# Performance work log

Hardware: AMD Instinct MI355X
Metric: run time of the kernel (lower is better)

Reference implementation:

```python
import jax, jax.numpy as jnp
import numpy as np

N = 100000          # nodes per node type (paper, author)
E = 250000          # edges per relation
D_IN = 128          # input feature dim
H, C = 4, 32        # heads, channels per head (h_dim = H*C = 128)
HD = H * C
OUT = 349           # num classes
RELS = ["c", "w", "wb"]  # cites(paper->paper), writes(author->paper), written_by(paper->author)


def setup_inputs() -> dict:
    key = jax.random.key(0)
    ks = iter(jax.random.split(key, 64))
    def nrm(shape, scale=0.1):
        return jax.random.normal(next(ks), shape, jnp.float32) * scale
    inp = {
        "x_paper": jax.random.normal(next(ks), (N, D_IN), jnp.float32),
        "x_author": jax.random.normal(next(ks), (N, D_IN), jnp.float32),
        "ei_cites": jax.random.randint(next(ks), (2, E), 0, N),
        "ei_writes": jax.random.randint(next(ks), (2, E), 0, N),
        "ei_written": jax.random.randint(next(ks), (2, E), 0, N),
    }
    for l, din in [(0, D_IN), (1, HD)]:
        for r in RELS:
            inp[f"W{l}_{r}"] = nrm((din, HD))
            inp[f"as{l}_{r}"] = nrm((H, C))
            inp[f"ad{l}_{r}"] = nrm((H, C))
            inp[f"b{l}_{r}"] = jnp.zeros((HD,), jnp.float32)
    inp["lin_W"] = nrm((HD, OUT))
    inp["lin_b"] = jnp.zeros((OUT,), jnp.float32)
    return inp


def _gat_conv(x_src, x_dst, ei, W, att_s, att_d, b, n_dst):
    """PyG GATConv (concat heads, add_self_loops=False, shared lin for src/dst)."""
    h_s = (x_src @ W).reshape(-1, H, C)              # [Ns,H,C]
    h_d = (x_dst @ W).reshape(-1, H, C)              # [Nd,H,C]
    a_s = (h_s * att_s).sum(-1)                      # [Ns,H]
    a_d = (h_d * att_d).sum(-1)                      # [Nd,H]
    src, dst = ei[0], ei[1]
    e = jax.nn.leaky_relu(a_s[src] + a_d[dst], 0.2)  # [E,H]
    # segment softmax over incoming edges per dst node
    m = jax.ops.segment_max(e, dst, num_segments=n_dst)
    m = jnp.where(jnp.isfinite(m), m, 0.0)
    w = jnp.exp(e - m[dst])
    z = jax.ops.segment_sum(w, dst, num_segments=n_dst)
    alpha = w / (z[dst] + 1e-16)                     # [E,H]
    msg = h_s[src] * alpha[..., None]                # [E,H,C]
    agg = jax.ops.segment_sum(msg, dst, num_segments=n_dst)
    return agg.reshape(n_dst, HD) + b


def _forward(x_paper, x_author, ei_cites, ei_writes, ei_written, params, lin_W, lin_b):
    xp, xa = x_paper, x_author
    for l in range(2):
        p = params[l]
        # HeteroConv with sum aggregation across relations per dst node type
        op = _gat_conv(xp, xp, ei_cites, *p["c"], N) + _gat_conv(xa, xp, ei_writes, *p["w"], N)
        oa = _gat_conv(xp, xa, ei_written, *p["wb"], N)
        xp, xa = op, oa
        if l != 1:
            xp = jax.nn.leaky_relu(xp, 0.01)  # F.leaky_relu default slope
            xa = jax.nn.leaky_relu(xa, 0.01)
            # dropout: identity in eval/reference mode
    return xp @ lin_W + lin_b  # [N, OUT]


def reference(x_paper, x_author,
              W0_c, as0_c, ad0_c, b0_c, W0_w, as0_w, ad0_w, b0_w, W0_wb, as0_wb, ad0_wb, b0_wb,
              W1_c, as1_c, ad1_c, b1_c, W1_w, as1_w, ad1_w, b1_w, W1_wb, as1_wb, ad1_wb, b1_wb,
              lin_W, lin_b, ei_cites, ei_writes, ei_written):
    params = [
        {"c": (W0_c, as0_c, ad0_c, b0_c), "w": (W0_w, as0_w, ad0_w, b0_w), "wb": (W0_wb, as0_wb, ad0_wb, b0_wb)},
        {"c": (W1_c, as1_c, ad1_c, b1_c), "w": (W1_w, as1_w, ad1_w, b1_w), "wb": (W1_wb, as1_wb, ad1_wb, b1_wb)},
    ]
    return _forward(x_paper, x_author, ei_cites, ei_writes, ei_written, params, lin_W, lin_b)
```

## Files before the change

kernel.cpp:

```cpp
#include <hip/hip_runtime.h>

#define NN 100000
#define EE 250000
#define CAP 32

typedef unsigned int u32;
typedef unsigned short ushort;
typedef __attribute__((ext_vector_type(8))) short bf16x8;
typedef __attribute__((ext_vector_type(4))) float f32x4;

__device__ __forceinline__ ushort f2bf(float x) {
    u32 u = __float_as_uint(x);
    return (ushort)((u + 0x7fffu + ((u >> 16) & 1u)) >> 16);
}
__device__ __forceinline__ float bf2f(ushort h) {
    return __uint_as_float(((u32)h) << 16);
}

__global__ __launch_bounds__(256) void gemm_att(
    const float* __restrict__ X, const float* __restrict__ W,
    const float* __restrict__ atts, const float* __restrict__ attd,
    float* __restrict__ H, float* __restrict__ aS, float* __restrict__ aD)
{
    __shared__ float sW[64 * 128];
    __shared__ float sXT[128 * 32];
    const int tid = threadIdx.x;
    const size_t r0 = (size_t)blockIdx.x * 32;

    {
        int rl = tid & 31, kg = tid >> 5;
        const float4* Xr = (const float4*)(X + (r0 + rl) * 128);
#pragma unroll
        for (int t = 0; t < 4; ++t) {
            float4 u = Xr[kg * 4 + t];
            int k = kg * 16 + t * 4;
            sXT[(k + 0) * 32 + rl] = u.x;
            sXT[(k + 1) * 32 + rl] = u.y;
            sXT[(k + 2) * 32 + rl] = u.z;
            sXT[(k + 3) * 32 + rl] = u.w;
        }
    }

    const int jg = tid & 31;
    const int rg = tid >> 5;
    float acc[4][4] = {};

    for (int kh = 0; kh < 2; ++kh) {
        __syncthreads();
        const float4* Wu = (const float4*)(W + kh * 64 * 128);
        float4* sWv = (float4*)sW;
#pragma unroll
        for (int t = 0; t < 8; ++t)
            sWv[tid + 256 * t] = Wu[tid + 256 * t];
        __syncthreads();
#pragma unroll 4
        for (int k = 0; k < 64; ++k) {
            const float4 w = ((const float4*)sW)[k * 32 + jg];
            const int kk = kh * 64 + k;
            const float4 x = ((const float4*)sXT)[kk * 8 + rg];
            acc[0][0] += w.x * x.x; acc[0][1] += w.y * x.x; acc[0][2] += w.z * x.x; acc[0][3] += w.w * x.x;
            acc[1][0] += w.x * x.y; acc[1][1] += w.y * x.y; acc[1][2] += w.z * x.y; acc[1][3] += w.w * x.y;
            acc[2][0] += w.x * x.z; acc[2][1] += w.y * x.z; acc[2][2] += w.z * x.z; acc[2][3] += w.w * x.z;
            acc[3][0] += w.x * x.w; acc[3][1] += w.y * x.w; acc[3][2] += w.z * x.w; acc[3][3] += w.w * x.w;
        }
    }

    const float4 sv = ((const float4*)atts)[jg];
    const float4 dv = ((const float4*)attd)[jg];
    const int h = jg >> 3;

#pragma unroll
    for (int i = 0; i < 4; ++i) {
        const size_t row = r0 + rg * 4 + i;
        if (H)
            ((float4*)H)[row * 32 + jg] = make_float4(acc[i][0], acc[i][1], acc[i][2], acc[i][3]);
        float ps = acc[i][0] * sv.x + acc[i][1] * sv.y + acc[i][2] * sv.z + acc[i][3] * sv.w;
        float pd = acc[i][0] * dv.x + acc[i][1] * dv.y + acc[i][2] * dv.z + acc[i][3] * dv.w;
        ps += __shfl_xor(ps, 1); ps += __shfl_xor(ps, 2); ps += __shfl_xor(ps, 4);
        pd += __shfl_xor(pd, 1); pd += __shfl_xor(pd, 2); pd += __shfl_xor(pd, 4);
        if ((jg & 7) == 0) {
            aS[row * 4 + h] = ps;
            aD[row * 4 + h] = pd;
        }
    }
}

__global__ __launch_bounds__(256) void fold_w3(
    const float* __restrict__ W0, const float* __restrict__ a0,
    const float* __restrict__ W1, const float* __restrict__ a1,
    const float* __restrict__ W2, const float* __restrict__ a2,
    float* __restrict__ Wf)
{
    int i = blockIdx.x * 256 + threadIdx.x;
    if (i >= 1536) return;
    int r = i >> 9, j = i & 511;
    int k = j >> 2, h = j & 3;
    const float* W = (r == 0) ? W0 : (r == 1) ? W1 : W2;
    const float* a = (r == 0) ? a0 : (r == 1) ? a1 : a2;
    float s = 0.f;
#pragma unroll
    for (int c = 0; c < 32; ++c)
        s += W[k * 128 + h * 32 + c] * a[h * 32 + c];
    Wf[i] = s;
}

__global__ __launch_bounds__(256) void gemv_att(
    const float* __restrict__ X, const float* __restrict__ Wf,
    float* __restrict__ aD)
{
    __shared__ float sWf[512];
    const int tid = threadIdx.x;
    if (tid < 128)
        ((float4*)sWf)[tid] = ((const float4*)Wf)[tid];
    __syncthreads();
    const int t = blockIdx.x * 256 + tid;
    const int n = t >> 5, lane = t & 31;
    if (n >= NN) return;
    const float4 x = ((const float4*)X)[(size_t)n * 32 + lane];
    const float4 w0 = ((const float4*)sWf)[lane * 4 + 0];
    const float4 w1 = ((const float4*)sWf)[lane * 4 + 1];
    const float4 w2 = ((const float4*)sWf)[lane * 4 + 2];
    const float4 w3 = ((const float4*)sWf)[lane * 4 + 3];
    float p0 = x.x * w0.x + x.y * w1.x + x.z * w2.x + x.w * w3.x;
    float p1 = x.x * w0.y + x.y * w1.y + x.z * w2.y + x.w * w3.y;
    float p2 = x.x * w0.z + x.y * w1.z + x.z * w2.z + x.w * w3.z;
    float p3 = x.x * w0.w + x.y * w1.w + x.z * w2.w + x.w * w3.w;
#pragma unroll
    for (int off = 1; off < 32; off <<= 1) {
        p0 += __shfl_xor(p0, off);
        p1 += __shfl_xor(p1, off);
        p2 += __shfl_xor(p2, off);
        p3 += __shfl_xor(p3, off);
    }
    if (lane == 0)
        ((float4*)aD)[n] = make_float4(p0, p1, p2, p3);
}

__global__ __launch_bounds__(256) void fill_buckets(
    const int* __restrict__ ei, int* __restrict__ deg, int* __restrict__ bkt)
{
    int e = blockIdx.x * 256 + threadIdx.x;
    if (e >= EE) return;
    int s = ei[e], d = ei[EE + e];
    int slot = atomicAdd(&deg[d], 1);
    if (slot >= 0 && slot < CAP) bkt[(size_t)d * CAP + slot] = s;
}

__global__ __launch_bounds__(256) void aggregate(
    const int* __restrict__ deg, const int* __restrict__ bkt,
    const float* __restrict__ aS, const float* __restrict__ aD,
    const float* __restrict__ Hs, float* __restrict__ out,
    int accumulate, const float* __restrict__ b1, const float* __restrict__ b2,
    int act)
{
    int t = blockIdx.x * 256 + threadIdx.x;
    int d = t >> 5, lane = t & 31;
    if (d >= NN) return;
    int g = deg[d]; if (g > CAP) g = CAP; if (g < 0) g = 0;
    const int h = lane >> 3;
    const float adh = aD[d * 4 + h];
    const int* mybkt = bkt + (size_t)d * CAP;

    const int4 sa = *(const int4*)mybkt;
    const int4 sb = *(const int4*)(mybkt + 4);
    int sidx[8] = {sa.x, sa.y, sa.z, sa.w, sb.x, sb.y, sb.z, sb.w};
#pragma unroll
    for (int j = 0; j < 8; ++j)
        sidx[j] = (j < g) ? sidx[j] : 0;

    float e[8];
#pragma unroll
    for (int j = 0; j < 8; ++j) {
        float ev = aS[sidx[j] * 4 + h] + adh;
        e[j] = ev > 0.f ? ev : 0.2f * ev;
    }
    float m = -INFINITY;
#pragma unroll
    for (int j = 0; j < 8; ++j)
        if (j < g) m = fmaxf(m, e[j]);
    for (int j = 8; j < g; ++j) {
        int s = mybkt[j];
        float ev = aS[s * 4 + h] + adh;
        ev = ev > 0.f ? ev : 0.2f * ev;
        m = fmaxf(m, ev);
    }

    float4 acc = make_float4(0.f, 0.f, 0.f, 0.f);
    float z = 0.f;
#pragma unroll
    for (int j = 0; j < 8; ++j) {
        if (j < g) {
            float w = __expf(e[j] - m);
            z += w;
            float4 hv = ((const float4*)Hs)[(size_t)sidx[j] * 32 + lane];
            acc.x += w * hv.x; acc.y += w * hv.y; acc.z += w * hv.z; acc.w += w * hv.w;
        }
    }
    for (int j = 8; j < g; ++j) {
        int s = mybkt[j];
        float ev = aS[s * 4 + h] + adh;
        ev = ev > 0.f ? ev : 0.2f * ev;
        float w = __expf(ev - m);
        z += w;
        float4 hv = ((const float4*)Hs)[(size_t)s * 32 + lane];
        acc.x += w * hv.x; acc.y += w * hv.y; acc.z += w * hv.z; acc.w += w * hv.w;
    }
    float inv = 1.f / (z + 1e-16f);
    acc.x *= inv; acc.y *= inv; acc.z *= inv; acc.w *= inv;

    if (accumulate) {
        float4 p = ((const float4*)out)[(size_t)d * 32 + lane];
        acc.x += p.x; acc.y += p.y; acc.z += p.z; acc.w += p.w;
    }
    if (b1) {
        float4 bv = ((const float4*)b1)[lane];
        acc.x += bv.x; acc.y += bv.y; acc.z += bv.z; acc.w += bv.w;
    }
    if (b2) {
        float4 bv = ((const float4*)b2)[lane];
        acc.x += bv.x; acc.y += bv.y; acc.z += bv.z; acc.w += bv.w;
    }
    if (act) {
        acc.x = acc.x > 0.f ? acc.x : 0.01f * acc.x;
        acc.y = acc.y > 0.f ? acc.y : 0.01f * acc.y;
        acc.z = acc.z > 0.f ? acc.z : 0.01f * acc.z;
        acc.w = acc.w > 0.f ? acc.w : 0.01f * acc.w;
    }
    ((float4*)out)[(size_t)d * 32 + lane] = acc;
}

__global__ __launch_bounds__(256) void pad_w(
    const float* __restrict__ Wl, const float* __restrict__ bl,
    ushort* __restrict__ Whi, ushort* __restrict__ Wlo, float* __restrict__ bp)
{
    int i = blockIdx.x * 256 + threadIdx.x;
    if (i >= 384 * 128) return;
    int n = i >> 7, k = i & 127;
    float w = (n < 349) ? Wl[k * 349 + n] : 0.0f;
    ushort h = f2bf(w);
    Whi[i] = h;
    Wlo[i] = f2bf(w - bf2f(h));
    if (i < 384) bp[i] = (i < 349) ? bl[i] : 0.0f;
}

__global__ __launch_bounds__(256) void gemm_out(
    const float* __restrict__ X, const ushort* __restrict__ Whi,
    const ushort* __restrict__ Wlo, const float* __restrict__ bp,
    float* __restrict__ out)
{
    __shared__ ushort sAhi[64 * 128];
    __shared__ ushort sAlo[64 * 128];
    const int tid = threadIdx.x;
    const size_t r0 = (size_t)blockIdx.x * 64;

    {
        const int rl = tid >> 2, sub = tid & 3;
        const size_t row = r0 + rl;
        const float4* Xr = (const float4*)(X + row * 128);
        const u32 swz = ((u32)(rl & 7)) << 4;
        const float4 z4 = make_float4(0.f, 0.f, 0.f, 0.f);
#pragma unroll
        for (int i = 0; i < 4; ++i) {
            float4 u0 = (row < NN) ? Xr[sub * 8 + 2 * i] : z4;
            float4 u1 = (row < NN) ? Xr[sub * 8 + 2 * i + 1] : z4;
            float v[8] = {u0.x, u0.y, u0.z, u0.w, u1.x, u1.y, u1.z, u1.w};
            bf16x8 h8, l8;
#pragma unroll
            for (int e = 0; e < 8; ++e) {
                ushort h = f2bf(v[e]);
                h8[e] = (short)h;
                l8[e] = (short)f2bf(v[e] - bf2f(h));
            }
            u32 byteoff = ((u32)rl * 256u + (u32)((sub * 32 + i * 8) * 2)) ^ swz;
            *(bf16x8*)((char*)sAhi + byteoff) = h8;
            *(bf16x8*)((char*)sAlo + byteoff) = l8;
        }
    }
    __syncthreads();

    const int wave = tid >> 6, lane = tid & 63;
    const int lr = lane & 15;
    const int lg = lane >> 4;
    const int ncol0 = wave * 96;

    f32x4 acc[4][6];
#pragma unroll
    for (int mt = 0; mt < 4; ++mt)
#pragma unroll
        for (int nt = 0; nt < 6; ++nt)
            acc[mt][nt] = (f32x4){0.f, 0.f, 0.f, 0.f};

    for (int ks = 0; ks < 4; ++ks) {
        bf16x8 ah[4], al[4];
#pragma unroll
        for (int mt = 0; mt < 4; ++mt) {
            const int row = mt * 16 + lr;
            u32 byteoff = ((u32)row * 256u + (u32)(ks * 64 + lg * 16))
                          ^ (((u32)(row & 7)) << 4);
            ah[mt] = *(const bf16x8*)((const char*)sAhi + byteoff);
            al[mt] = *(const bf16x8*)((const char*)sAlo + byteoff);
        }
        bf16x8 bh[6], bl6[6];
#pragma unroll
        for (int nt = 0; nt < 6; ++nt) {
            const int n = ncol0 + nt * 16 + lr;
            const size_t off = (size_t)n * 128 + ks * 32 + lg * 8;
            bh[nt]  = *(const bf16x8*)(Whi + off);
            bl6[nt] = *(const bf16x8*)(Wlo + off);
        }
#pragma unroll
        for (int mt = 0; mt < 4; ++mt)
#pragma unroll
            for (int nt = 0; nt < 6; ++nt) {
                acc[mt][nt] = __builtin_amdgcn_mfma_f32_16x16x32_bf16(
                    ah[mt], bh[nt], acc[mt][nt], 0, 0, 0);
                acc[mt][nt] = __builtin_amdgcn_mfma_f32_16x16x32_bf16(
                    ah[mt], bl6[nt], acc[mt][nt], 0, 0, 0);
                acc[mt][nt] = __builtin_amdgcn_mfma_f32_16x16x32_bf16(
                    al[mt], bh[nt], acc[mt][nt], 0, 0, 0);
            }
    }

#pragma unroll
    for (int nt = 0; nt < 6; ++nt) {
        const int n = ncol0 + nt * 16 + lr;
        if (n >= 349) continue;
        const float bb = bp[n];
#pragma unroll
        for (int mt = 0; mt < 4; ++mt) {
#pragma unroll
            for (int r = 0; r < 4; ++r) {
                const size_t row = r0 + mt * 16 + lg * 4 + r;
                if (row < NN)
                    out[row * 349 + n] = acc[mt][nt][r] + bb;
            }
        }
    }
}

extern "C" void kernel_launch(void* const* d_in, const int* in_sizes, int n_in,
                              void* d_out, int out_size, void* d_ws, size_t ws_size,
                              hipStream_t stream)
{
    (void)in_sizes; (void)n_in; (void)out_size; (void)ws_size;
    const float* xp = (const float*)d_in[0];
    const float* xa = (const float*)d_in[1];
    const int* eic = (const int*)d_in[2];
    const int* eiw = (const int*)d_in[3];
    const int* eiwb = (const int*)d_in[4];
    auto Wl = [&](int l, int r) { return (const float*)d_in[5 + (l * 3 + r) * 4 + 0]; };
    auto As = [&](int l, int r) { return (const float*)d_in[5 + (l * 3 + r) * 4 + 1]; };
    auto Ad = [&](int l, int r) { return (const float*)d_in[5 + (l * 3 + r) * 4 + 2]; };
    auto Bs = [&](int l, int r) { return (const float*)d_in[5 + (l * 3 + r) * 4 + 3]; };
    const float* linW = (const float*)d_in[29];
    const float* linb = (const float*)d_in[30];

    char* wsp = (char*)d_ws;
    auto carve = [&](size_t bytes) -> void* {
        void* p = (void*)wsp;
        wsp += (bytes + 255) & ~(size_t)255;
        return p;
    };
    float* Hs = (float*)carve((size_t)NN * 128 * 4);
    float* P1 = (float*)carve((size_t)NN * 128 * 4);
    float* A1 = (float*)carve((size_t)NN * 128 * 4);
    float* P2 = (float*)carve((size_t)NN * 128 * 4);
    int* deg = (int*)carve((size_t)NN * 3 * 4);
    int* deg_c = deg, *deg_w = deg + NN, *deg_wb = deg + 2 * NN;
    int* bkt_c = (int*)carve((size_t)NN * CAP * 4);
    int* bkt_w = (int*)carve((size_t)NN * CAP * 4);
    int* bkt_wb = (int*)carve((size_t)NN * CAP * 4);
    float* aS = (float*)carve((size_t)NN * 4 * 4);
    float* aD = (float*)carve((size_t)NN * 4 * 4);
    float* aX = (float*)carve((size_t)NN * 4 * 4);
    ushort* Whi = (ushort*)carve((size_t)384 * 128 * 2);
    ushort* Wlo = (ushort*)carve((size_t)384 * 128 * 2);
    float* bp = (float*)carve((size_t)384 * 4);
    float* Wf = (float*)carve((size_t)3 * 512 * 4);

    dim3 blk(256);
    const int gG = NN / 32;
    const int gE = (EE + 255) / 256;
    const int gA = NN * 32 / 256;
    const int gO = (NN + 63) / 64;

    hipMemsetAsync(deg, 0, (size_t)NN * 3 * 4, stream);
    fill_buckets<<<gE, blk, 0, stream>>>(eic, deg_c, bkt_c);
    fill_buckets<<<gE, blk, 0, stream>>>(eiw, deg_w, bkt_w);
    fill_buckets<<<gE, blk, 0, stream>>>(eiwb, deg_wb, bkt_wb);
    fold_w3<<<6, blk, 0, stream>>>(Wl(0, 2), Ad(0, 2), Wl(0, 1), Ad(0, 1),
                                   Wl(1, 1), Ad(1, 1), Wf);

    gemm_att<<<gG, blk, 0, stream>>>(xp, Wl(0, 2), As(0, 2), Ad(0, 2), Hs, aS, aX);
    gemv_att<<<gA, blk, 0, stream>>>(xa, Wf + 0 * 512, aD);
    aggregate<<<gA, blk, 0, stream>>>(deg_wb, bkt_wb, aS, aD, Hs, A1, 0, Bs(0, 2), nullptr, 1);

    gemm_att<<<gG, blk, 0, stream>>>(xp, Wl(0, 0), As(0, 0), Ad(0, 0), Hs, aS, aD);
    aggregate<<<gA, blk, 0, stream>>>(deg_c, bkt_c, aS, aD, Hs, P1, 0, nullptr, nullptr, 0);

    gemm_att<<<gG, blk, 0, stream>>>(xa, Wl(0, 1), As(0, 1), Ad(0, 1), Hs, aS, aX);
    gemv_att<<<gA, blk, 0, stream>>>(xp, Wf + 1 * 512, aD);
    aggregate<<<gA, blk, 0, stream>>>(deg_w, bkt_w, aS, aD, Hs, P1, 1, Bs(0, 0), Bs(0, 1), 1);

    gemm_att<<<gG, blk, 0, stream>>>(P1, Wl(1, 0), As(1, 0), Ad(1, 0), Hs, aS, aD);
    aggregate<<<gA, blk, 0, stream>>>(deg_c, bkt_c, aS, aD, Hs, P2, 0, nullptr, nullptr, 0);

    gemm_att<<<gG, blk, 0, stream>>>(A1, Wl(1, 1), As(1, 1), Ad(1, 1), Hs, aS, aX);
    gemv_att<<<gA, blk, 0, stream>>>(P1, Wf + 2 * 512, aD);
    aggregate<<<gA, blk, 0, stream>>>(deg_w, bkt_w, aS, aD, Hs, P2, 1, Bs(1, 0), Bs(1, 1), 0);

    pad_w<<<192, blk, 0, stream>>>(linW, linb, Whi, Wlo, bp);
    gemm_out<<<gO, blk, 0, stream>>>(P2, Whi, Wlo, bp, (float*)d_out);
}
```

Baseline: 958.0 us.

## Fuse dual-relation paper aggregation and stage output GEMM stores through LDS

```diff
diff --git a/kernel.cpp b/kernel.cpp
--- a/kernel.cpp
+++ b/kernel.cpp
@@ -146,18 +146,13 @@
     if (slot >= 0 && slot < CAP) bkt[(size_t)d * CAP + slot] = s;
 }
 
-__global__ __launch_bounds__(256) void aggregate(
+__device__ __forceinline__ float4 agg_one(
+    int d, int lane, int h,
     const int* __restrict__ deg, const int* __restrict__ bkt,
     const float* __restrict__ aS, const float* __restrict__ aD,
-    const float* __restrict__ Hs, float* __restrict__ out,
-    int accumulate, const float* __restrict__ b1, const float* __restrict__ b2,
-    int act)
-{
-    int t = blockIdx.x * 256 + threadIdx.x;
-    int d = t >> 5, lane = t & 31;
-    if (d >= NN) return;
+    const float* __restrict__ Hs)
+{
     int g = deg[d]; if (g > CAP) g = CAP; if (g < 0) g = 0;
-    const int h = lane >> 3;
     const float adh = aD[d * 4 + h];
     const int* mybkt = bkt + (size_t)d * CAP;
 
@@ -207,16 +202,55 @@
     }
     float inv = 1.f / (z + 1e-16f);
     acc.x *= inv; acc.y *= inv; acc.z *= inv; acc.w *= inv;
-
-    if (accumulate) {
-        float4 p = ((const float4*)out)[(size_t)d * 32 + lane];
-        acc.x += p.x; acc.y += p.y; acc.z += p.z; acc.w += p.w;
-    }
+    return acc;
+}
+
+__global__ __launch_bounds__(256) void aggregate(
+    const int* __restrict__ deg, const int* __restrict__ bkt,
+    const float* __restrict__ aS, const float* __restrict__ aD,
+    const float* __restrict__ Hs, float* __restrict__ out,
+    const float* __restrict__ b1, int act)
+{
+    int t = blockIdx.x * 256 + threadIdx.x;
+    int d = t >> 5, lane = t & 31;
+    if (d >= NN) return;
+    const int h = lane >> 3;
+    float4 acc = agg_one(d, lane, h, deg, bkt, aS, aD, Hs);
     if (b1) {
         float4 bv = ((const float4*)b1)[lane];
         acc.x += bv.x; acc.y += bv.y; acc.z += bv.z; acc.w += bv.w;
     }
-    if (b2) {
+    if (act) {
+        acc.x = acc.x > 0.f ? acc.x : 0.01f * acc.x;
+        acc.y = acc.y > 0.f ? acc.y : 0.01f * acc.y;
+        acc.z = acc.z > 0.f ? acc.z : 0.01f * acc.z;
+        acc.w = acc.w > 0.f ? acc.w : 0.01f * acc.w;
+    }
+    ((float4*)out)[(size_t)d * 32 + lane] = acc;
+}
+
+__global__ __launch_bounds__(256) void aggregate2(
+    const int* __restrict__ deg_c, const int* __restrict__ bkt_c,
+    const float* __restrict__ aS_c, const float* __restrict__ aD_c,
+    const float* __restrict__ Hs_c,
+    const int* __restrict__ deg_w, const int* __restrict__ bkt_w,
+    const float* __restrict__ aS_w, const float* __restrict__ aD_w,
+    const float* __restrict__ Hs_w,
+    float* __restrict__ out,
+    const float* __restrict__ b1, const float* __restrict__ b2, int act)
+{
+    int t = blockIdx.x * 256 + threadIdx.x;
+    int d = t >> 5, lane = t & 31;
+    if (d >= NN) return;
+    const int h = lane >> 3;
+    float4 acc_c = agg_one(d, lane, h, deg_c, bkt_c, aS_c, aD_c, Hs_c);
+    float4 acc  = agg_one(d, lane, h, deg_w, bkt_w, aS_w, aD_w, Hs_w);
+    acc.x += acc_c.x; acc.y += acc_c.y; acc.z += acc_c.z; acc.w += acc_c.w;
+    {
+        float4 bv = ((const float4*)b1)[lane];
+        acc.x += bv.x; acc.y += bv.y; acc.z += bv.z; acc.w += bv.w;
+    }
+    {
         float4 bv = ((const float4*)b2)[lane];
         acc.x += bv.x; acc.y += bv.y; acc.z += bv.z; acc.w += bv.w;
     }
@@ -248,21 +282,21 @@
     const ushort* __restrict__ Wlo, const float* __restrict__ bp,
     float* __restrict__ out)
 {
-    __shared__ ushort sAhi[64 * 128];
-    __shared__ ushort sAlo[64 * 128];
+    __shared__ __align__(16) char smem[22400];
+    ushort* sAhi = (ushort*)smem;
+    ushort* sAlo = (ushort*)(smem + 8192);
+    float*  sOut = (float*)smem;
     const int tid = threadIdx.x;
-    const size_t r0 = (size_t)blockIdx.x * 64;
+    const size_t r0 = (size_t)blockIdx.x * 32;
 
     {
-        const int rl = tid >> 2, sub = tid & 3;
-        const size_t row = r0 + rl;
-        const float4* Xr = (const float4*)(X + row * 128);
+        const int rl = tid >> 3, sub = tid & 7;
+        const float4* Xr = (const float4*)(X + (r0 + rl) * 128);
         const u32 swz = ((u32)(rl & 7)) << 4;
-        const float4 z4 = make_float4(0.f, 0.f, 0.f, 0.f);
-#pragma unroll
-        for (int i = 0; i < 4; ++i) {
-            float4 u0 = (row < NN) ? Xr[sub * 8 + 2 * i] : z4;
-            float4 u1 = (row < NN) ? Xr[sub * 8 + 2 * i + 1] : z4;
+#pragma unroll
+        for (int i = 0; i < 2; ++i) {
+            float4 u0 = Xr[sub * 4 + 2 * i];
+            float4 u1 = Xr[sub * 4 + 2 * i + 1];
             float v[8] = {u0.x, u0.y, u0.z, u0.w, u1.x, u1.y, u1.z, u1.w};
             bf16x8 h8, l8;
 #pragma unroll
@@ -271,7 +305,7 @@
                 h8[e] = (short)h;
                 l8[e] = (short)f2bf(v[e] - bf2f(h));
             }
-            u32 byteoff = ((u32)rl * 256u + (u32)((sub * 32 + i * 8) * 2)) ^ swz;
+            u32 byteoff = (((u32)rl * 256u) + (u32)(sub * 32 + i * 16)) ^ swz;
             *(bf16x8*)((char*)sAhi + byteoff) = h8;
             *(bf16x8*)((char*)sAlo + byteoff) = l8;
         }
@@ -283,57 +317,60 @@
     const int lg = lane >> 4;
     const int ncol0 = wave * 96;
 
-    f32x4 acc[4][6];
-#pragma unroll
-    for (int mt = 0; mt < 4; ++mt)
+    f32x4 acc[2][6];
+#pragma unroll
+    for (int mt = 0; mt < 2; ++mt)
 #pragma unroll
         for (int nt = 0; nt < 6; ++nt)
             acc[mt][nt] = (f32x4){0.f, 0.f, 0.f, 0.f};
 
     for (int ks = 0; ks < 4; ++ks) {
-        bf16x8 ah[4], al[4];
-#pragma unroll
-        for (int mt = 0; mt < 4; ++mt) {
+        bf16x8 ah[2], al[2];
+#pragma unroll
+        for (int mt = 0; mt < 2; ++mt) {
             const int row = mt * 16 + lr;
-            u32 byteoff = ((u32)row * 256u + (u32)(ks * 64 + lg * 16))
+            u32 byteoff = (((u32)row * 256u) + (u32)(ks * 64 + lg * 16))
                           ^ (((u32)(row & 7)) << 4);
             ah[mt] = *(const bf16x8*)((const char*)sAhi + byteoff);
             al[mt] = *(const bf16x8*)((const char*)sAlo + byteoff);
         }
-        bf16x8 bh[6], bl6[6];
 #pragma unroll
         for (int nt = 0; nt < 6; ++nt) {
             const int n = ncol0 + nt * 16 + lr;
             const size_t off = (size_t)n * 128 + ks * 32 + lg * 8;
-            bh[nt]  = *(const bf16x8*)(Whi + off);
-            bl6[nt] = *(const bf16x8*)(Wlo + off);
-        }
-#pragma unroll
-        for (int mt = 0; mt < 4; ++mt)
-#pragma unroll
-            for (int nt = 0; nt < 6; ++nt) {
+            const bf16x8 bh = *(const bf16x8*)(Whi + off);
+            const bf16x8 bl = *(const bf16x8*)(Wlo + off);
+#pragma unroll
+            for (int mt = 0; mt < 2; ++mt) {
                 acc[mt][nt] = __builtin_amdgcn_mfma_f32_16x16x32_bf16(
-                    ah[mt], bh[nt], acc[mt][nt], 0, 0, 0);
+                    ah[mt], bh, acc[mt][nt], 0, 0, 0);
                 acc[mt][nt] = __builtin_amdgcn_mfma_f32_16x16x32_bf16(
-                    ah[mt], bl6[nt], acc[mt][nt], 0, 0, 0);
+                    ah[mt], bl, acc[mt][nt], 0, 0, 0);
                 acc[mt][nt] = __builtin_amdgcn_mfma_f32_16x16x32_bf16(
-                    al[mt], bh[nt], acc[mt][nt], 0, 0, 0);
+                    al[mt], bh, acc[mt][nt], 0, 0, 0);
             }
-    }
-
-#pragma unroll
-    for (int nt = 0; nt < 6; ++nt) {
-        const int n = ncol0 + nt * 16 + lr;
-        if (n >= 349) continue;
-        const float bb = bp[n];
-#pragma unroll
-        for (int mt = 0; mt < 4; ++mt) {
-#pragma unroll
-            for (int r = 0; r < 4; ++r) {
-                const size_t row = r0 + mt * 16 + lg * 4 + r;
-                if (row < NN)
-                    out[row * 349 + n] = acc[mt][nt][r] + bb;
+        }
+    }
+    __syncthreads();
+
+    for (int mt = 0; mt < 2; ++mt) {
+        if (mt) __syncthreads();
+#pragma unroll
+        for (int nt = 0; nt < 6; ++nt) {
+            const int n = ncol0 + nt * 16 + lr;
+            if (n < 349) {
+                const float bb = bp[n];
+#pragma unroll
+                for (int r = 0; r < 4; ++r)
+                    sOut[(lg * 4 + r) * 349 + n] = acc[mt][nt][r] + bb;
             }
+        }
+        __syncthreads();
+        {
+            float4* dst = (float4*)(out + (r0 + (size_t)mt * 16) * 349);
+            const float4* src = (const float4*)sOut;
+            for (int i = tid; i < 1396; i += 256)
+                dst[i] = src[i];
         }
     }
 }
@@ -372,6 +409,8 @@
     int* bkt_wb = (int*)carve((size_t)NN * CAP * 4);
     float* aS = (float*)carve((size_t)NN * 4 * 4);
     float* aD = (float*)carve((size_t)NN * 4 * 4);
+    float* aS2 = (float*)carve((size_t)NN * 4 * 4);
+    float* aD2 = (float*)carve((size_t)NN * 4 * 4);
     float* aX = (float*)carve((size_t)NN * 4 * 4);
     ushort* Whi = (ushort*)carve((size_t)384 * 128 * 2);
     ushort* Wlo = (ushort*)carve((size_t)384 * 128 * 2);
@@ -382,7 +421,6 @@
     const int gG = NN / 32;
     const int gE = (EE + 255) / 256;
     const int gA = NN * 32 / 256;
-    const int gO = (NN + 63) / 64;
 
     hipMemsetAsync(deg, 0, (size_t)NN * 3 * 4, stream);
     fill_buckets<<<gE, blk, 0, stream>>>(eic, deg_c, bkt_c);
@@ -393,22 +431,22 @@
 
     gemm_att<<<gG, blk, 0, stream>>>(xp, Wl(0, 2), As(0, 2), Ad(0, 2), Hs, aS, aX);
     gemv_att<<<gA, blk, 0, stream>>>(xa, Wf + 0 * 512, aD);
-    aggregate<<<gA, blk, 0, stream>>>(deg_wb, bkt_wb, aS, aD, Hs, A1, 0, Bs(0, 2), nullptr, 1);
+    aggregate<<<gA, blk, 0, stream>>>(deg_wb, bkt_wb, aS, aD, Hs, A1, Bs(0, 2), 1);
 
     gemm_att<<<gG, blk, 0, stream>>>(xp, Wl(0, 0), As(0, 0), Ad(0, 0), Hs, aS, aD);
-    aggregate<<<gA, blk, 0, stream>>>(deg_c, bkt_c, aS, aD, Hs, P1, 0, nullptr, nullptr, 0);
-
-    gemm_att<<<gG, blk, 0, stream>>>(xa, Wl(0, 1), As(0, 1), Ad(0, 1), Hs, aS, aX);
-    gemv_att<<<gA, blk, 0, stream>>>(xp, Wf + 1 * 512, aD);
-    aggregate<<<gA, blk, 0, stream>>>(deg_w, bkt_w, aS, aD, Hs, P1, 1, Bs(0, 0), Bs(0, 1), 1);
+    gemm_att<<<gG, blk, 0, stream>>>(xa, Wl(0, 1), As(0, 1), Ad(0, 1), P2, aS2, aX);
+    gemv_att<<<gA, blk, 0, stream>>>(xp, Wf + 1 * 512, aD2);
+    aggregate2<<<gA, blk, 0, stream>>>(deg_c, bkt_c, aS, aD, Hs,
+                                       deg_w, bkt_w, aS2, aD2, P2,
+                                       P1, Bs(0, 0), Bs(0, 1), 1);
 
     gemm_att<<<gG, blk, 0, stream>>>(P1, Wl(1, 0), As(1, 0), Ad(1, 0), Hs, aS, aD);
-    aggregate<<<gA, blk, 0, stream>>>(deg_c, bkt_c, aS, aD, Hs, P2, 0, nullptr, nullptr, 0);
-
-    gemm_att<<<gG, blk, 0, stream>>>(A1, Wl(1, 1), As(1, 1), Ad(1, 1), Hs, aS, aX);
-    gemv_att<<<gA, blk, 0, stream>>>(P1, Wf + 2 * 512, aD);
-    aggregate<<<gA, blk, 0, stream>>>(deg_w, bkt_w, aS, aD, Hs, P2, 1, Bs(1, 0), Bs(1, 1), 0);
+    gemm_att<<<gG, blk, 0, stream>>>(A1, Wl(1, 1), As(1, 1), Ad(1, 1), A1, aS2, aX);
+    gemv_att<<<gA, blk, 0, stream>>>(P1, Wf + 2 * 512, aD2);
+    aggregate2<<<gA, blk, 0, stream>>>(deg_c, bkt_c, aS, aD, Hs,
+                                       deg_w, bkt_w, aS2, aD2, A1,
+                                       P2, Bs(1, 0), Bs(1, 1), 0);
 
     pad_w<<<192, blk, 0, stream>>>(linW, linb, Whi, Wlo, bp);
-    gemm_out<<<gO, blk, 0, stream>>>(P2, Whi, Wlo, bp, (float*)d_out);
-}
+    gemm_out<<<gG, blk, 0, stream>>>(P2, Whi, Wlo, bp, (float*)d_out);
+}
```

Result: faster. 879.9 us (-8.1%).
